# Optimization experiments

Hardware: AMD Instinct MI355X
Metric: run time of the kernel (lower is better)

The kernel has to match this reference:

```python
import jax, jax.numpy as jnp
import numpy as np
from jax import lax

EPS = 1e-6
DT_RANK = 24  # ceil(384/16), Mamba convention
D_STATE = 16


def _ln(x, g, b, eps=EPS):
    m = jnp.mean(x, axis=-1, keepdims=True)
    v = jnp.mean((x - m) ** 2, axis=-1, keepdims=True)
    return (x - m) * lax.rsqrt(v + eps) * g + b


def setup_inputs() -> dict:
    key = jax.random.key(0)
    ks = jax.random.split(key, 10)
    B, Dd, Hh, Ww, C = 2, 8, 16, 16, 384
    di, ds, r = 384, D_STATE, DT_RANK  # d_inner = expand * d_model = 384
    s = 0.02
    f = lambda k, shape: (jax.random.normal(k, shape, jnp.float32) * s)
    return {
        "x": jax.random.normal(ks[0], (B, Dd, Hh, Ww, C), jnp.float32),
        "g1": jnp.ones((C,), jnp.float32), "b1": jnp.zeros((C,), jnp.float32),
        "W_in": f(ks[1], (C, 2 * di)), "b_in": jnp.zeros((2 * di,), jnp.float32),
        "conv_w": f(ks[2], (di, 1, 3, 3, 3)), "conv_b": jnp.zeros((di,), jnp.float32),
        "W_x": f(ks[3], (di, r + 2 * ds)),
        "W_dt": f(ks[4], (r, di)), "b_dt": jnp.zeros((di,), jnp.float32),
        "A_log": jnp.tile(jnp.log(jnp.arange(1, ds + 1, dtype=jnp.float32)), (di, 1)),
        "D_skip": jnp.ones((di,), jnp.float32),
        "on_g": jnp.ones((di,), jnp.float32), "on_b": jnp.zeros((di,), jnp.float32),
        "W_out": f(ks[5], (di, C)), "b_out": jnp.zeros((C,), jnp.float32),
        "g2": jnp.ones((C,), jnp.float32), "b2": jnp.zeros((C,), jnp.float32),
        "W1": f(ks[6], (C, C)), "b1m": jnp.zeros((C,), jnp.float32),
        "W2": f(ks[7], (C, C)), "b2m": jnp.zeros((C,), jnp.float32),
    }


def _ss3d(h, W_in, b_in, conv_w, conv_b, W_x, W_dt, b_dt, A_log, D_skip, on_g, on_b, W_out, b_out):
    # h: [B, D, H, W, C] -> Mamba-style selective scan over flattened DHW (orientation 0)
    B, Dd, Hh, Ww, C = h.shape
    di = W_in.shape[1] // 2
    ds = D_STATE
    L = Dd * Hh * Ww
    seq = h.reshape(B, L, C)
    xz = seq @ W_in + b_in                      # [B, L, 2*di]
    xin, z = jnp.split(xz, 2, axis=-1)
    # depthwise 3D conv + SiLU on the x branch
    xc = xin.reshape(B, Dd, Hh, Ww, di).transpose(0, 4, 1, 2, 3)  # [B, di, D, H, W]
    xc = lax.conv_general_dilated(xc, conv_w, (1, 1, 1), 'SAME',
                                  feature_group_count=di,
                                  dimension_numbers=('NCDHW', 'OIDHW', 'NCDHW'))
    xc = xc + conv_b[None, :, None, None, None]
    xin = jax.nn.silu(xc).transpose(0, 2, 3, 4, 1).reshape(B, L, di)
    # input-dependent dt, B, C
    dbc = xin @ W_x                              # [B, L, r + 2*ds]
    dt, Bm, Cm = jnp.split(dbc, [DT_RANK, DT_RANK + ds], axis=-1)
    dt = jax.nn.softplus(dt @ W_dt + b_dt)       # [B, L, di]
    A = -jnp.exp(A_log)                          # [di, ds]
    dA = jnp.exp(dt[..., None] * A)              # [B, L, di, ds]
    dBx = dt[..., None] * Bm[:, :, None, :] * xin[..., None]  # [B, L, di, ds]

    def step(carry, inp):
        da, dbx, c = inp                         # [B,di,ds], [B,di,ds], [B,ds]
        carry = da * carry + dbx
        y = jnp.einsum('bds,bs->bd', carry, c)
        return carry, y

    xs = (dA.transpose(1, 0, 2, 3), dBx.transpose(1, 0, 2, 3), Cm.transpose(1, 0, 2))
    h0 = jnp.zeros((B, di, ds), dA.dtype)
    _, ys = lax.scan(step, h0, xs)               # ys: [L, B, di]
    y = ys.transpose(1, 0, 2) + xin * D_skip
    y = _ln(y, on_g, on_b) * jax.nn.silu(z)
    out = y @ W_out + b_out
    return out.reshape(B, Dd, Hh, Ww, C)


def reference(x, g1, b1, W_in, b_in, conv_w, conv_b, W_x, W_dt, b_dt, A_log, D_skip,
              on_g, on_b, W_out, b_out, g2, b2, W1, b1m, W2, b2m):
    # x + SS3D(LN(x)); then x + MLP(LN(x)).  drop_path/dropout = 0 (eval)
    a = _ss3d(_ln(x, g1, b1), W_in, b_in, conv_w, conv_b, W_x, W_dt, b_dt,
              A_log, D_skip, on_g, on_b, W_out, b_out)
    x1 = x + a
    h2 = _ln(x1, g2, b2)
    mlp = jax.nn.gelu(h2 @ W1 + b1m) @ W2 + b2m
    return x1 + mlp
```

## Files before the change

### kernel.cpp

```cpp
#include <hip/hip_runtime.h>
#include <hip/hip_bf16.h>

using bf16 = __hip_bfloat16;
#define DEV __device__ __forceinline__

typedef __attribute__((ext_vector_type(8))) short short8;
typedef __attribute__((ext_vector_type(8))) unsigned short ushort8;
typedef __attribute__((ext_vector_type(4))) float f32x4;

constexpr int Bb = 2, DD = 8, HH = 16, WW = 16;
constexpr int C = 384, DI = 384, DS = 16, RR = 24;
constexpr int L = DD * HH * WW;
constexpr int M = Bb * L;

DEV bf16 f2b(float v) { return __float2bfloat16(v); }
DEV unsigned short f2bu(float v) {
    bf16 t = __float2bfloat16(v);
    unsigned short u; __builtin_memcpy(&u, &t, 2); return u;
}
DEV float braw(unsigned short u) {
    unsigned int x = ((unsigned int)u) << 16;
    float f; __builtin_memcpy(&f, &x, 4); return f;
}
DEV bool isbf(const unsigned short* g1p) { return g1p[0] == 0x3F80; }

typedef const __attribute__((address_space(1))) unsigned int* gaddr_t;
typedef __attribute__((address_space(3))) unsigned int* laddr_t;
DEV void gload_lds16(const void* g, void* l) {
    __builtin_amdgcn_global_load_lds((gaddr_t)g, (laddr_t)l, 16, 0, 0);
}

DEV float wred64(float v) {
    #pragma unroll
    for (int off = 32; off > 0; off >>= 1) v += __shfl_xor(v, off, 64);
    return v;
}
DEV float siluf(float x) { return x / (1.0f + __expf(-x)); }
DEV float softplusf(float x) { return (x > 15.0f) ? x : log1pf(__expf(x)); }
DEV float gelu_tanh(float x) {
    const float k0 = 0.7978845608028654f;
    float u = k0 * (x + 0.044715f * x * x * x);
    float e = __expf(2.0f * u);
    float t = 1.0f - 2.0f / (e + 1.0f);
    return 0.5f * x * (1.0f + t);
}

struct PrepTab {
    const void* tsrc[4];
    unsigned short* tdst[4];
    int tK[4], tN[4];
    const void* csrc[17];
    float* cdst[17];
    int coff[18];
};
__global__ __launch_bounds__(256) void prep_k(PrepTab t,
                                              const unsigned short* __restrict__ g1p,
                                              int ctotal) {
    bool fl = isbf(g1p);
    int z = blockIdx.z;
    if (z < 4) {
        __shared__ unsigned short tt[32][33];
        int N = t.tN[z], K = t.tK[z];
        int n0 = blockIdx.x * 32, k0 = blockIdx.y * 32;
        if (n0 >= N || k0 >= K) return;
        const void* src = t.tsrc[z];
        unsigned short* dst = t.tdst[z];
        int tx = threadIdx.x & 31, ty = threadIdx.x >> 5;
        #pragma unroll
        for (int i = 0; i < 4; i++) {
            int k = k0 + ty + i * 8;
            unsigned short u;
            if (fl) u = ((const unsigned short*)src)[(size_t)k * N + n0 + tx];
            else    u = f2bu(((const float*)src)[(size_t)k * N + n0 + tx]);
            tt[ty + i * 8][tx] = u;
        }
        __syncthreads();
        #pragma unroll
        for (int i = 0; i < 4; i++) {
            int n = n0 + ty + i * 8;
            dst[(size_t)n * K + k0 + tx] = tt[tx][ty + i * 8];
        }
    } else {
        int i = (blockIdx.y * 24 + blockIdx.x) * 256 + threadIdx.x;
        if (i >= ctotal) return;
        int seg = 0;
        #pragma unroll
        for (int k = 1; k < 18; k++) seg += (i >= t.coff[k]) ? 1 : 0;
        int j = i - t.coff[seg];
        const void* s = t.csrc[seg];
        float v = fl ? braw(((const unsigned short*)s)[j]) : ((const float*)s)[j];
        t.cdst[seg][j] = v;
    }
}

template <bool RAWIN>
__global__ __launch_bounds__(256) void ln_k(const void* __restrict__ xr,
                                            const float* __restrict__ g,
                                            const float* __restrict__ b,
                                            bf16* __restrict__ out,
                                            const unsigned short* __restrict__ g1p) {
    bool fl = RAWIN ? isbf(g1p) : false;
    int wave = blockIdx.x * 4 + (threadIdx.x >> 6);
    int lane = threadIdx.x & 63;
    size_t base = (size_t)wave * C;
    float v[6];
    #pragma unroll
    for (int j = 0; j < 6; j++) {
        size_t idx = base + lane + 64 * j;
        if (RAWIN && fl) v[j] = braw(((const unsigned short*)xr)[idx]);
        else             v[j] = ((const float*)xr)[idx];
    }
    float s = 0.f;
    #pragma unroll
    for (int j = 0; j < 6; j++) s += v[j];
    s = wred64(s);
    float mean = s * (1.0f / C);
    float q = 0.f;
    #pragma unroll
    for (int j = 0; j < 6; j++) { float d = v[j] - mean; q += d * d; }
    q = wred64(q);
    float rstd = rsqrtf(q * (1.0f / C) + 1e-6f);
    #pragma unroll
    for (int j = 0; j < 6; j++) {
        int c = lane + 64 * j;
        out[base + c] = f2b((v[j] - mean) * rstd * g[c] + b[c]);
    }
}

enum { EPI_XZT = 0, EPI_OUT = 1, EPI_GELU = 2, EPI_FINAL = 3 };

template <int N, int TN, int EPI>
__global__ __launch_bounds__(256) void gemm_mfma(const bf16* __restrict__ A,
                                                 const unsigned short* __restrict__ Bt,
                                                 const float* __restrict__ bias,
                                                 float* __restrict__ o0,
                                                 float* __restrict__ o1,
                                                 const float* __restrict__ auxf,
                                                 const void* __restrict__ auxraw,
                                                 void* __restrict__ obf,
                                                 const unsigned short* __restrict__ g1p) {
    __shared__ unsigned short Asb[128 * 32];
    __shared__ unsigned short Bsb[TN * 32];
    constexpr int MT = (TN == 128) ? 4 : 2;
    int tid = threadIdx.x;
    int m0 = blockIdx.x * 128, n0 = blockIdx.y * TN;
    int wid = tid >> 6, lane = tid & 63;
    int wm = (TN == 128) ? (wid >> 1) * 64 : wid * 32;
    int wn = (TN == 128) ? (wid & 1) * 64 : 0;
    int quad = lane >> 4, l15 = lane & 15;
    f32x4 acc[MT][4] = {};
    int srow = tid >> 2, sseg = (tid & 3) * 8;
    const unsigned short* Au = (const unsigned short*)A;
    for (int k0 = 0; k0 < 384; k0 += 32) {
        __syncthreads();
        gload_lds16(Au + (size_t)(m0 + srow) * 384 + k0 + sseg,
                    &Asb[srow * 32 + sseg]);
        gload_lds16(Au + (size_t)(m0 + 64 + srow) * 384 + k0 + sseg,
                    &Asb[(64 + srow) * 32 + sseg]);
        gload_lds16(Bt + (size_t)(n0 + srow) * 384 + k0 + sseg,
                    &Bsb[srow * 32 + sseg]);
        if constexpr (TN == 128)
            gload_lds16(Bt + (size_t)(n0 + 64 + srow) * 384 + k0 + sseg,
                        &Bsb[(64 + srow) * 32 + sseg]);
        __syncthreads();
        short8 af[MT], bfr[4];
        #pragma unroll
        for (int mt = 0; mt < MT; mt++)
            af[mt] = *(const short8*)&Asb[(wm + mt * 16 + l15) * 32 + quad * 8];
        #pragma unroll
        for (int nt = 0; nt < 4; nt++)
            bfr[nt] = *(const short8*)&Bsb[(wn + nt * 16 + l15) * 32 + quad * 8];
        #pragma unroll
        for (int mt = 0; mt < MT; mt++)
            #pragma unroll
            for (int nt = 0; nt < 4; nt++)
                acc[mt][nt] = __builtin_amdgcn_mfma_f32_16x16x32_bf16(
                    af[mt], bfr[nt], acc[mt][nt], 0, 0, 0);
    }
    bool fl = (EPI == EPI_FINAL || EPI == EPI_OUT) ? isbf(g1p) : false;
    #pragma unroll
    for (int mt = 0; mt < MT; mt++) {
        #pragma unroll
        for (int nt = 0; nt < 4; nt++) {
            int n = n0 + wn + nt * 16 + l15;
            int mb = m0 + wm + mt * 16 + quad * 4;
            float bi = bias[n];
            if constexpr (EPI == EPI_XZT) {
                f32x4 v = acc[mt][nt];
                v[0] += bi; v[1] += bi; v[2] += bi; v[3] += bi;
                float* dst = (n < 384) ? (o0 + (size_t)n * M + mb)
                                       : (o1 + (size_t)(n - 384) * M + mb);
                *(f32x4*)dst = v;
            } else {
                #pragma unroll
                for (int r = 0; r < 4; r++) {
                    int m = mb + r;
                    float v = acc[mt][nt][r] + bi;
                    if constexpr (EPI == EPI_OUT) {
                        float av;
                        if (fl) av = braw(((const unsigned short*)auxraw)[(size_t)m * 384 + n]);
                        else    av = ((const float*)auxraw)[(size_t)m * 384 + n];
                        o0[(size_t)m * 384 + n] = v + av;
                    } else if constexpr (EPI == EPI_GELU) {
                        ((bf16*)obf)[(size_t)m * 384 + n] = f2b(gelu_tanh(v));
                    } else {
                        float rr = v + auxf[(size_t)m * 384 + n];
                        if (fl) ((bf16*)obf)[(size_t)m * 384 + n] = f2b(rr);
                        else    ((float*)obf)[(size_t)m * 384 + n] = rr;
                    }
                }
            }
        }
    }
}

__global__ __launch_bounds__(256) void convT_k(const float* __restrict__ xT,
                                               const float* __restrict__ cw,
                                               const float* __restrict__ cb,
                                               float* __restrict__ xinT) {
    int c = blockIdx.y;
    int m0 = (blockIdx.x * 256 + threadIdx.x) * 4;
    int l = m0 & (L - 1);
    int d = l >> 8, h = (l >> 4) & 15, w0 = l & 15;
    const float* xc = xT + (size_t)c * M;
    const float* wc = cw + c * 27;
    float bias = cb[c];
    float acc[4] = {bias, bias, bias, bias};
    #pragma unroll
    for (int kd = -1; kd <= 1; kd++) {
        int dd = d + kd; if ((unsigned)dd >= 8u) continue;
        #pragma unroll
        for (int kh = -1; kh <= 1; kh++) {
            int hh = h + kh; if ((unsigned)hh >= 16u) continue;
            int mm = m0 + kd * 256 + kh * 16;
            float vv[6];
            vv[0] = (w0 == 0) ? 0.f : xc[mm - 1];
            float4 v14 = *(const float4*)(xc + mm);
            vv[1] = v14.x; vv[2] = v14.y; vv[3] = v14.z; vv[4] = v14.w;
            vv[5] = (w0 == 12) ? 0.f : xc[mm + 4];
            const float* wk = wc + (kd + 1) * 9 + (kh + 1) * 3;
            float wa = wk[0], wb = wk[1], wcc = wk[2];
            #pragma unroll
            for (int j = 0; j < 4; j++)
                acc[j] = fmaf(vv[j], wa, fmaf(vv[j + 1], wb, fmaf(vv[j + 2], wcc, acc[j])));
        }
    }
    float4 o = make_float4(siluf(acc[0]), siluf(acc[1]), siluf(acc[2]), siluf(acc[3]));
    *(float4*)(xinT + (size_t)c * M + m0) = o;
}

__global__ __launch_bounds__(256) void dbc2_k(const float* __restrict__ xinT,
                                              const float* __restrict__ Wx,
                                              float* __restrict__ part) {
    __shared__ float As[16][64];
    __shared__ float Ws[16 * 56];
    int tid = threadIdx.x;
    int m0 = blockIdx.x * 64;
    int kc = blockIdx.y;
    int tm = tid & 63, grp = tid >> 6;
    int kk = tid >> 4, mc = (tid & 15) * 4;
    float acc[14] = {};
    for (int k0 = kc * 64; k0 < kc * 64 + 64; k0 += 16) {
        float4 av = *(const float4*)(xinT + (size_t)(k0 + kk) * M + m0 + mc);
        __syncthreads();
        *(float4*)&As[kk][mc] = av;
        for (int idx = tid; idx < 16 * 56; idx += 256)
            Ws[idx] = Wx[k0 * 56 + idx];
        __syncthreads();
        #pragma unroll
        for (int k = 0; k < 16; k++) {
            float a = As[k][tm];
            #pragma unroll
            for (int jj = 0; jj < 14; jj++)
                acc[jj] = fmaf(a, Ws[k * 56 + grp * 14 + jj], acc[jj]);
        }
    }
    int m = m0 + tm;
    #pragma unroll
    for (int jj = 0; jj < 14; jj++) {
        int col = grp * 14 + jj;
        part[((size_t)kc * 56 + col) * M + m] = acc[jj];
    }
}

__global__ __launch_bounds__(256) void dbcred_k(const float* __restrict__ part,
                                                float* __restrict__ dtrT,
                                                unsigned short* __restrict__ Brow,
                                                unsigned short* __restrict__ Crow) {
    int col = blockIdx.y;
    int m = blockIdx.x * 256 + threadIdx.x;
    float s = 0.f;
    #pragma unroll
    for (int kc = 0; kc < 6; kc++)
        s += part[((size_t)kc * 56 + col) * M + m];
    if (col < 24)      dtrT[(size_t)col * M + m] = s;
    else if (col < 40) Brow[(size_t)m * 16 + col - 24] = f2bu(s);
    else               Crow[(size_t)m * 16 + col - 40] = f2bu(s);
}

__global__ __launch_bounds__(256) void dtT_k(const float* __restrict__ dtrT,
                                             const float* __restrict__ Wdt,
                                             const float* __restrict__ bdt,
                                             float* __restrict__ dtT) {
    int lane = threadIdx.x & 63;
    int wv = threadIdx.x >> 6;
    int n = blockIdx.y * 4 + wv;
    int m = blockIdx.x * 64 + lane;
    float acc = bdt[n];
    #pragma unroll
    for (int j = 0; j < 24; j++)
        acc = fmaf(dtrT[(size_t)j * M + m], Wdt[j * 384 + n], acc);
    dtT[(size_t)n * M + m] = softplusf(acc);
}

__global__ __launch_bounds__(128) void scan4_k(const float* __restrict__ dtT,
                                               const float* __restrict__ xinT,
                                               const unsigned short* __restrict__ Brow,
                                               const unsigned short* __restrict__ Crow,
                                               const float* __restrict__ alog,
                                               const float* __restrict__ dsk,
                                               float* __restrict__ yT) {
    __shared__ float dt_s[2112], x_s[2112];
    __shared__ float ypart[2 * 2112];
    int bi = blockIdx.x;
    int b = bi / DI, d = bi % DI;
    int wave = threadIdx.x >> 6, lane = threadIdx.x & 63;
    int s0 = wave * 8;
    float Aneg[8];
    #pragma unroll
    for (int ss = 0; ss < 8; ss++) Aneg[ss] = -__expf(alog[d * DS + s0 + ss]);
    const float* dtp = dtT + (size_t)d * M + b * L;
    const float* xp  = xinT + (size_t)d * M + b * L;
    #pragma unroll
    for (int i = 0; i < 4; i++) {
        int t4 = (threadIdx.x + i * 128) * 4;
        float4 dv = *(const float4*)(dtp + t4);
        float4 xv = *(const float4*)(xp + t4);
        int base = t4 + (t4 >> 5);
        dt_s[base + 0] = dv.x; dt_s[base + 1] = dv.y;
        dt_s[base + 2] = dv.z; dt_s[base + 3] = dv.w;
        x_s[base + 0] = xv.x; x_s[base + 1] = xv.y;
        x_s[base + 2] = xv.z; x_s[base + 3] = xv.w;
    }
    __syncthreads();
    const unsigned short* Bp = Brow + ((size_t)b * L) * 16 + s0;
    const unsigned short* Cp = Crow + ((size_t)b * L) * 16 + s0;
    int tbase = lane * 32;
    int pbase = lane * 33;
    float Ap[8], Bg[8];
    #pragma unroll
    for (int ss = 0; ss < 8; ss++) { Ap[ss] = 1.f; Bg[ss] = 0.f; }
    #pragma unroll 4
    for (int j = 0; j < 32; j++) {
        float dtv = dt_s[pbase + j];
        float dxv = dtv * x_s[pbase + j];
        ushort8 bu = *(const ushort8*)(Bp + (size_t)(tbase + j) * 16);
        #pragma unroll
        for (int ss = 0; ss < 8; ss++) {
            float dA = __expf(dtv * Aneg[ss]);
            Bg[ss] = fmaf(dA, Bg[ss], dxv * braw(bu[ss]));
            Ap[ss] *= dA;
        }
    }
    float carry[8];
    #pragma unroll
    for (int ss = 0; ss < 8; ss++) {
        float a = Ap[ss], bb = Bg[ss];
        #pragma unroll
        for (int off = 1; off < 64; off <<= 1) {
            float ap = __shfl_up(a, off, 64);
            float bp = __shfl_up(bb, off, 64);
            if (lane >= off) { bb = fmaf(a, bp, bb); a *= ap; }
        }
        float c = __shfl_up(bb, 1, 64);
        carry[ss] = (lane == 0) ? 0.f : c;
    }
    float* ypw = ypart + wave * 2112;
    float h[8];
    #pragma unroll
    for (int ss = 0; ss < 8; ss++) h[ss] = carry[ss];
    #pragma unroll 4
    for (int j = 0; j < 32; j++) {
        float dtv = dt_s[pbase + j];
        float dxv = dtv * x_s[pbase + j];
        size_t toff = (size_t)(tbase + j) * 16;
        ushort8 bu = *(const ushort8*)(Bp + toff);
        ushort8 cu = *(const ushort8*)(Cp + toff);
        float acc = 0.f;
        #pragma unroll
        for (int ss = 0; ss < 8; ss++) {
            float dA = __expf(dtv * Aneg[ss]);
            h[ss] = fmaf(dA, h[ss], dxv * braw(bu[ss]));
            acc = fmaf(h[ss], braw(cu[ss]), acc);
        }
        ypw[pbase + j] = acc;
    }
    __syncthreads();
    float Dv = dsk[d];
    float* yp = yT + (size_t)d * M + b * L;
    #pragma unroll
    for (int i = 0; i < 16; i++) {
        int t = threadIdx.x + 128 * i;
        int ti = t + (t >> 5);
        yp[t] = fmaf(x_s[ti], Dv, ypart[ti] + ypart[2112 + ti]);
    }
}

__global__ __launch_bounds__(256) void lnmulT_k(const float* __restrict__ yT,
                                                const float* __restrict__ zT,
                                                const float* __restrict__ g,
                                                const float* __restrict__ b,
                                                unsigned short* __restrict__ yact) {
    __shared__ float rs1[8][32], rs2[8][32];
    __shared__ float meanb[32], rstdb[32];
    __shared__ unsigned short tile[32][392];
    int moff = threadIdx.x & 31;
    int dsub = threadIdx.x >> 5;
    int m0 = blockIdx.x * 32;
    size_t mg = m0 + moff;
    float s1 = 0.f, s2 = 0.f;
    #pragma unroll 8
    for (int j = 0; j < 48; j++) {
        int d = dsub + 8 * j;
        float v = yT[(size_t)d * M + mg];
        s1 += v; s2 += v * v;
    }
    rs1[dsub][moff] = s1;
    rs2[dsub][moff] = s2;
    __syncthreads();
    if (threadIdx.x < 32) {
        float a1 = 0.f, a2 = 0.f;
        #pragma unroll
        for (int ss = 0; ss < 8; ss++) { a1 += rs1[ss][threadIdx.x]; a2 += rs2[ss][threadIdx.x]; }
        float mean = a1 * (1.0f / DI);
        float var = a2 * (1.0f / DI) - mean * mean;
        meanb[threadIdx.x] = mean;
        rstdb[threadIdx.x] = rsqrtf(var + 1e-6f);
    }
    __syncthreads();
    float mean = meanb[moff], rstd = rstdb[moff];
    #pragma unroll 8
    for (int j = 0; j < 48; j++) {
        int d = dsub + 8 * j;
        float v = yT[(size_t)d * M + mg];
        float ln = (v - mean) * rstd * g[d] + b[d];
        float zv = zT[(size_t)d * M + mg];
        tile[moff][d] = f2bu(ln * siluf(zv));
    }
    __syncthreads();
    #pragma unroll
    for (int i = 0; i < 6; i++) {
        int chunk = threadIdx.x + 256 * i;
        int row = chunk / 48, cc = chunk % 48;
        *(uint4*)(yact + ((size_t)(m0 + row)) * 384 + cc * 8) =
            *(const uint4*)&tile[row][cc * 8];
    }
}

extern "C" void kernel_launch(void* const* d_in, const int* in_sizes, int n_in,
                              void* d_out, int out_size, void* d_ws, size_t ws_size,
                              hipStream_t stream) {
    float* ws = (float*)d_ws;
    constexpr size_t S = (size_t)M * 384;
    bf16*  hb   = (bf16*)ws;
    float* xT   = ws + S / 2;
    float* zT   = xT + S;
    float* xinT = zT + S;
    float* dtT  = xinT + S;
    float* x1   = dtT + S;
    float* dtrT = x1 + S;
    unsigned short* Brow = (unsigned short*)(dtrT + (size_t)24 * M);
    unsigned short* Crow = Brow + (size_t)M * 16;
    float* part = (float*)(Crow + (size_t)M * 16);
    float* smalls = part + (size_t)6 * 56 * M;

    float* g1f  = smalls;        float* b1f  = g1f + 384;
    float* binf = b1f + 384;     float* cwf  = binf + 768;
    float* cbf  = cwf + 10368;   float* wxf  = cbf + 384;
    float* wdtf = wxf + 21504;   float* bdtf = wdtf + 9216;
    float* alogf= bdtf + 384;    float* dskf = alogf + 6144;
    float* ongf = dskf + 384;    float* onbf = ongf + 384;
    float* boutf= onbf + 384;    float* g2f  = boutf + 384;
    float* b2f_ = g2f + 384;     float* b1mf = b2f_ + 384;
    float* b2mf = b1mf + 384;
    unsigned short* WinT  = (unsigned short*)(b2mf + 384);
    unsigned short* WoutT = WinT + 294912;
    unsigned short* W1T   = WoutT + 147456;
    unsigned short* W2T   = W1T + 147456;

    float* yT = xT;
    bf16* h2b = hb;
    unsigned short* yactb = (unsigned short*)dtT;
    unsigned short* m1b = (unsigned short*)zT;
    const unsigned short* g1p = (const unsigned short*)d_in[1];

    PrepTab tab;
    {
        tab.tsrc[0] = d_in[3];  tab.tdst[0] = WinT;  tab.tK[0] = 384; tab.tN[0] = 768;
        tab.tsrc[1] = d_in[14]; tab.tdst[1] = WoutT; tab.tK[1] = 384; tab.tN[1] = 384;
        tab.tsrc[2] = d_in[18]; tab.tdst[2] = W1T;   tab.tK[2] = 384; tab.tN[2] = 384;
        tab.tsrc[3] = d_in[20]; tab.tdst[3] = W2T;   tab.tK[3] = 384; tab.tN[3] = 384;
        int idxs[17] = {1, 2, 4, 5, 6, 7, 8, 9, 10, 11, 12, 13, 15, 16, 17, 19, 21};
        float* dsts[17] = {g1f, b1f, binf, cwf, cbf, wxf, wdtf, bdtf, alogf, dskf,
                           ongf, onbf, boutf, g2f, b2f_, b1mf, b2mf};
        int ns[17] = {384, 384, 768, 10368, 384, 21504, 9216, 384, 6144, 384,
                      384, 384, 384, 384, 384, 384, 384};
        int off = 0;
        for (int k = 0; k < 17; k++) {
            tab.csrc[k] = d_in[idxs[k]];
            tab.cdst[k] = dsts[k];
            tab.coff[k] = off;
            off += ns[k];
        }
        tab.coff[17] = off;
        prep_k<<<dim3(24, 12, 5), 256, 0, stream>>>(tab, g1p, off);
    }

    ln_k<true><<<M / 4, 256, 0, stream>>>(d_in[0], g1f, b1f, hb, g1p);
    gemm_mfma<768, 128, EPI_XZT><<<dim3(M / 128, 6), 256, 0, stream>>>(
        hb, WinT, binf, xT, zT, nullptr, nullptr, nullptr, g1p);
    convT_k<<<dim3(M / 1024, DI), 256, 0, stream>>>(xT, cwf, cbf, xinT);
    dbc2_k<<<dim3(M / 64, 6), 256, 0, stream>>>(xinT, wxf, part);
    dbcred_k<<<dim3(M / 256, 56), 256, 0, stream>>>(part, dtrT, Brow, Crow);
    dtT_k<<<dim3(M / 64, DI / 4), 256, 0, stream>>>(dtrT, wdtf, bdtf, dtT);
    scan4_k<<<Bb * DI, 128, 0, stream>>>(dtT, xinT, Brow, Crow, alogf, dskf, yT);
    lnmulT_k<<<M / 32, 256, 0, stream>>>(yT, zT, ongf, onbf, yactb);
    gemm_mfma<384, 64, EPI_OUT><<<dim3(M / 128, 6), 256, 0, stream>>>(
        (const bf16*)yactb, WoutT, boutf, x1, nullptr, nullptr, d_in[0], nullptr, g1p);
    ln_k<false><<<M / 4, 256, 0, stream>>>(x1, g2f, b2f_, h2b, g1p);
    gemm_mfma<384, 64, EPI_GELU><<<dim3(M / 128, 6), 256, 0, stream>>>(
        h2b, W1T, b1mf, nullptr, nullptr, nullptr, nullptr, m1b, g1p);
    gemm_mfma<384, 64, EPI_FINAL><<<dim3(M / 128, 6), 256, 0, stream>>>(
        (const bf16*)m1b, W2T, b2mf, nullptr, nullptr, x1, nullptr, d_out, g1p);
}
```

Before: 230.6 us.

## Fuse LayerNorms into following GEMMs and merge dt reduction with dt projection

Removes both standalone LayerNorm kernels. Each GEMM that consumes normalized activations now computes per-row mean and rstd for its 128-row tile, then normalizes and converts the A operand to bf16 while staging it into shared memory. The split-K reduction of the x-projection partials is merged with the dt projection and softplus into one kernel, which drops the dtrT intermediate buffer and two kernel launches. In exchange, every N-tile block recomputes the row statistics and rereads the fp32 A rows (6x redundant reads). The A-tile loads are also now synchronous register loads instead of direct-to-LDS loads.

```diff
diff --git a/kernel.cpp b/kernel.cpp
--- a/kernel.cpp
+++ b/kernel.cpp
@@ -93,48 +93,131 @@
     }
 }
 
-template <bool RAWIN>
-__global__ __launch_bounds__(256) void ln_k(const void* __restrict__ xr,
-                                            const float* __restrict__ g,
-                                            const float* __restrict__ b,
-                                            bf16* __restrict__ out,
-                                            const unsigned short* __restrict__ g1p) {
-    bool fl = RAWIN ? isbf(g1p) : false;
-    int wave = blockIdx.x * 4 + (threadIdx.x >> 6);
-    int lane = threadIdx.x & 63;
-    size_t base = (size_t)wave * C;
-    float v[6];
-    #pragma unroll
-    for (int j = 0; j < 6; j++) {
-        size_t idx = base + lane + 64 * j;
-        if (RAWIN && fl) v[j] = braw(((const unsigned short*)xr)[idx]);
-        else             v[j] = ((const float*)xr)[idx];
-    }
-    float s = 0.f;
-    #pragma unroll
-    for (int j = 0; j < 6; j++) s += v[j];
-    s = wred64(s);
-    float mean = s * (1.0f / C);
-    float q = 0.f;
-    #pragma unroll
-    for (int j = 0; j < 6; j++) { float d = v[j] - mean; q += d * d; }
-    q = wred64(q);
-    float rstd = rsqrtf(q * (1.0f / C) + 1e-6f);
-    #pragma unroll
-    for (int j = 0; j < 6; j++) {
-        int c = lane + 64 * j;
-        out[base + c] = f2b((v[j] - mean) * rstd * g[c] + b[c]);
-    }
-}
-
 enum { EPI_XZT = 0, EPI_OUT = 1, EPI_GELU = 2, EPI_FINAL = 3 };
+
+template <int N, int TN, int EPI, bool ARAW>
+__global__ __launch_bounds__(256) void lngemm_k(const void* __restrict__ Ar,
+                                                const float* __restrict__ g,
+                                                const float* __restrict__ b,
+                                                const unsigned short* __restrict__ Bt,
+                                                const float* __restrict__ bias,
+                                                float* __restrict__ o0,
+                                                float* __restrict__ o1,
+                                                void* __restrict__ obf,
+                                                const unsigned short* __restrict__ g1p) {
+    __shared__ unsigned short Asb[128 * 32];
+    __shared__ unsigned short Bsb[TN * 32];
+    __shared__ float mean_s[128], rstd_s[128];
+    __shared__ float gb[768];
+    constexpr int MT = (TN == 128) ? 4 : 2;
+    int tid = threadIdx.x;
+    int m0 = blockIdx.x * 128, n0 = blockIdx.y * TN;
+    int wid = tid >> 6, lane = tid & 63;
+    bool fl = ARAW ? isbf(g1p) : false;
+    for (int i = tid; i < 384; i += 256) { gb[i] = g[i]; gb[384 + i] = b[i]; }
+    for (int r = 0; r < 32; r++) {
+        int row = m0 + wid * 32 + r;
+        float v[6];
+        #pragma unroll
+        for (int j = 0; j < 6; j++) {
+            size_t idx = (size_t)row * 384 + lane + 64 * j;
+            if (ARAW && fl) v[j] = braw(((const unsigned short*)Ar)[idx]);
+            else            v[j] = ((const float*)Ar)[idx];
+        }
+        float s = 0.f;
+        #pragma unroll
+        for (int j = 0; j < 6; j++) s += v[j];
+        s = wred64(s);
+        float mean = s * (1.0f / 384.0f);
+        float q = 0.f;
+        #pragma unroll
+        for (int j = 0; j < 6; j++) { float d = v[j] - mean; q += d * d; }
+        q = wred64(q);
+        if (lane == 0) {
+            mean_s[wid * 32 + r] = mean;
+            rstd_s[wid * 32 + r] = rsqrtf(q * (1.0f / 384.0f) + 1e-6f);
+        }
+    }
+    int wm = (TN == 128) ? (wid >> 1) * 64 : wid * 32;
+    int wn = (TN == 128) ? (wid & 1) * 64 : 0;
+    int quad = lane >> 4, l15 = lane & 15;
+    f32x4 acc[MT][4] = {};
+    int srow = tid >> 2, sseg = (tid & 3) * 8;
+    for (int k0 = 0; k0 < 384; k0 += 32) {
+        __syncthreads();
+        #pragma unroll
+        for (int half = 0; half < 2; half++) {
+            int r = srow + half * 64;
+            size_t off = (size_t)(m0 + r) * 384 + k0 + sseg;
+            float vals[8];
+            if (ARAW && fl) {
+                uint4 u = *(const uint4*)((const unsigned short*)Ar + off);
+                unsigned short us[8]; __builtin_memcpy(us, &u, 16);
+                #pragma unroll
+                for (int j = 0; j < 8; j++) vals[j] = braw(us[j]);
+            } else {
+                float4 f0 = *(const float4*)((const float*)Ar + off);
+                float4 f1 = *(const float4*)((const float*)Ar + off + 4);
+                vals[0] = f0.x; vals[1] = f0.y; vals[2] = f0.z; vals[3] = f0.w;
+                vals[4] = f1.x; vals[5] = f1.y; vals[6] = f1.z; vals[7] = f1.w;
+            }
+            float mn = mean_s[r], rs = rstd_s[r];
+            unsigned short ou[8];
+            #pragma unroll
+            for (int j = 0; j < 8; j++)
+                ou[j] = f2bu((vals[j] - mn) * rs * gb[k0 + sseg + j] + gb[384 + k0 + sseg + j]);
+            uint4 pk; __builtin_memcpy(&pk, ou, 16);
+            *(uint4*)&Asb[r * 32 + sseg] = pk;
+        }
+        gload_lds16(Bt + (size_t)(n0 + srow) * 384 + k0 + sseg, &Bsb[srow * 32 + sseg]);
+        if constexpr (TN == 128)
+            gload_lds16(Bt + (size_t)(n0 + 64 + srow) * 384 + k0 + sseg,
+                        &Bsb[(64 + srow) * 32 + sseg]);
+        __syncthreads();
+        short8 af[MT], bfr[4];
+        #pragma unroll
+        for (int mt = 0; mt < MT; mt++)
+            af[mt] = *(const short8*)&Asb[(wm + mt * 16 + l15) * 32 + quad * 8];
+        #pragma unroll
+        for (int nt = 0; nt < 4; nt++)
+            bfr[nt] = *(const short8*)&Bsb[(wn + nt * 16 + l15) * 32 + quad * 8];
+        #pragma unroll
+        for (int mt = 0; mt < MT; mt++)
+            #pragma unroll
+            for (int nt = 0; nt < 4; nt++)
+                acc[mt][nt] = __builtin_amdgcn_mfma_f32_16x16x32_bf16(
+                    af[mt], bfr[nt], acc[mt][nt], 0, 0, 0);
+    }
+    #pragma unroll
+    for (int mt = 0; mt < MT; mt++) {
+        #pragma unroll
+        for (int nt = 0; nt < 4; nt++) {
+            int n = n0 + wn + nt * 16 + l15;
+            int mb = m0 + wm + mt * 16 + quad * 4;
+            float bi = bias[n];
+            if constexpr (EPI == EPI_XZT) {
+                f32x4 v = acc[mt][nt];
+                v[0] += bi; v[1] += bi; v[2] += bi; v[3] += bi;
+                float* dst = (n < 384) ? (o0 + (size_t)n * M + mb)
+                                       : (o1 + (size_t)(n - 384) * M + mb);
+                *(f32x4*)dst = v;
+            } else {
+                #pragma unroll
+                for (int r = 0; r < 4; r++) {
+                    int m = mb + r;
+                    float v = acc[mt][nt][r] + bi;
+                    ((bf16*)obf)[(size_t)m * 384 + n] = f2b(gelu_tanh(v));
+                }
+            }
+        }
+    }
+}
 
 template <int N, int TN, int EPI>
 __global__ __launch_bounds__(256) void gemm_mfma(const bf16* __restrict__ A,
                                                  const unsigned short* __restrict__ Bt,
                                                  const float* __restrict__ bias,
                                                  float* __restrict__ o0,
-                                                 float* __restrict__ o1,
                                                  const float* __restrict__ auxf,
                                                  const void* __restrict__ auxraw,
                                                  void* __restrict__ obf,
@@ -153,12 +236,10 @@
     const unsigned short* Au = (const unsigned short*)A;
     for (int k0 = 0; k0 < 384; k0 += 32) {
         __syncthreads();
-        gload_lds16(Au + (size_t)(m0 + srow) * 384 + k0 + sseg,
-                    &Asb[srow * 32 + sseg]);
+        gload_lds16(Au + (size_t)(m0 + srow) * 384 + k0 + sseg, &Asb[srow * 32 + sseg]);
         gload_lds16(Au + (size_t)(m0 + 64 + srow) * 384 + k0 + sseg,
                     &Asb[(64 + srow) * 32 + sseg]);
-        gload_lds16(Bt + (size_t)(n0 + srow) * 384 + k0 + sseg,
-                    &Bsb[srow * 32 + sseg]);
+        gload_lds16(Bt + (size_t)(n0 + srow) * 384 + k0 + sseg, &Bsb[srow * 32 + sseg]);
         if constexpr (TN == 128)
             gload_lds16(Bt + (size_t)(n0 + 64 + srow) * 384 + k0 + sseg,
                         &Bsb[(64 + srow) * 32 + sseg]);
@@ -177,7 +258,7 @@
                 acc[mt][nt] = __builtin_amdgcn_mfma_f32_16x16x32_bf16(
                     af[mt], bfr[nt], acc[mt][nt], 0, 0, 0);
     }
-    bool fl = (EPI == EPI_FINAL || EPI == EPI_OUT) ? isbf(g1p) : false;
+    bool fl = isbf(g1p);
     #pragma unroll
     for (int mt = 0; mt < MT; mt++) {
         #pragma unroll
@@ -185,29 +266,19 @@
             int n = n0 + wn + nt * 16 + l15;
             int mb = m0 + wm + mt * 16 + quad * 4;
             float bi = bias[n];
-            if constexpr (EPI == EPI_XZT) {
-                f32x4 v = acc[mt][nt];
-                v[0] += bi; v[1] += bi; v[2] += bi; v[3] += bi;
-                float* dst = (n < 384) ? (o0 + (size_t)n * M + mb)
-                                       : (o1 + (size_t)(n - 384) * M + mb);
-                *(f32x4*)dst = v;
-            } else {
-                #pragma unroll
-                for (int r = 0; r < 4; r++) {
-                    int m = mb + r;
-                    float v = acc[mt][nt][r] + bi;
-                    if constexpr (EPI == EPI_OUT) {
-                        float av;
-                        if (fl) av = braw(((const unsigned short*)auxraw)[(size_t)m * 384 + n]);
-                        else    av = ((const float*)auxraw)[(size_t)m * 384 + n];
-                        o0[(size_t)m * 384 + n] = v + av;
-                    } else if constexpr (EPI == EPI_GELU) {
-                        ((bf16*)obf)[(size_t)m * 384 + n] = f2b(gelu_tanh(v));
-                    } else {
-                        float rr = v + auxf[(size_t)m * 384 + n];
-                        if (fl) ((bf16*)obf)[(size_t)m * 384 + n] = f2b(rr);
-                        else    ((float*)obf)[(size_t)m * 384 + n] = rr;
-                    }
+            #pragma unroll
+            for (int r = 0; r < 4; r++) {
+                int m = mb + r;
+                float v = acc[mt][nt][r] + bi;
+                if constexpr (EPI == EPI_OUT) {
+                    float av;
+                    if (fl) av = braw(((const unsigned short*)auxraw)[(size_t)m * 384 + n]);
+                    else    av = ((const float*)auxraw)[(size_t)m * 384 + n];
+                    o0[(size_t)m * 384 + n] = v + av;
+                } else {
+                    float rr = v + auxf[(size_t)m * 384 + n];
+                    if (fl) ((bf16*)obf)[(size_t)m * 384 + n] = f2b(rr);
+                    else    ((float*)obf)[(size_t)m * 384 + n] = rr;
                 }
             }
         }
@@ -283,34 +354,47 @@
     }
 }
 
-__global__ __launch_bounds__(256) void dbcred_k(const float* __restrict__ part,
-                                                float* __restrict__ dtrT,
+__global__ __launch_bounds__(256) void dbcfin_k(const float* __restrict__ part,
+                                                const float* __restrict__ Wdt,
+                                                const float* __restrict__ bdt,
+                                                float* __restrict__ dtT,
                                                 unsigned short* __restrict__ Brow,
                                                 unsigned short* __restrict__ Crow) {
-    int col = blockIdx.y;
-    int m = blockIdx.x * 256 + threadIdx.x;
-    float s = 0.f;
-    #pragma unroll
-    for (int kc = 0; kc < 6; kc++)
-        s += part[((size_t)kc * 56 + col) * M + m];
-    if (col < 24)      dtrT[(size_t)col * M + m] = s;
-    else if (col < 40) Brow[(size_t)m * 16 + col - 24] = f2bu(s);
-    else               Crow[(size_t)m * 16 + col - 40] = f2bu(s);
-}
-
-__global__ __launch_bounds__(256) void dtT_k(const float* __restrict__ dtrT,
-                                             const float* __restrict__ Wdt,
-                                             const float* __restrict__ bdt,
-                                             float* __restrict__ dtT) {
-    int lane = threadIdx.x & 63;
-    int wv = threadIdx.x >> 6;
-    int n = blockIdx.y * 4 + wv;
-    int m = blockIdx.x * 64 + lane;
-    float acc = bdt[n];
-    #pragma unroll
-    for (int j = 0; j < 24; j++)
-        acc = fmaf(dtrT[(size_t)j * M + m], Wdt[j * 384 + n], acc);
-    dtT[(size_t)n * M + m] = softplusf(acc);
+    __shared__ float dtr[24][64];
+    int tid = threadIdx.x;
+    int m0 = blockIdx.x * 64;
+    int ng = blockIdx.y;
+    for (int i = tid; i < 24 * 64; i += 256) {
+        int col = i >> 6, mm = i & 63;
+        float s = 0.f;
+        #pragma unroll
+        for (int kc = 0; kc < 6; kc++)
+            s += part[((size_t)kc * 56 + col) * M + m0 + mm];
+        dtr[col][mm] = s;
+    }
+    if (ng == 0) {
+        for (int i = tid; i < 32 * 64; i += 256) {
+            int col = 24 + (i >> 6), mm = i & 63;
+            float s = 0.f;
+            #pragma unroll
+            for (int kc = 0; kc < 6; kc++)
+                s += part[((size_t)kc * 56 + col) * M + m0 + mm];
+            int m = m0 + mm;
+            if (col < 40) Brow[(size_t)m * 16 + col - 24] = f2bu(s);
+            else          Crow[(size_t)m * 16 + col - 40] = f2bu(s);
+        }
+    }
+    __syncthreads();
+    int mm = tid & 63, nq = tid >> 6;
+    #pragma unroll 4
+    for (int nj = 0; nj < 16; nj++) {
+        int n = ng * 64 + nq * 16 + nj;
+        float acc = bdt[n];
+        #pragma unroll
+        for (int j = 0; j < 24; j++)
+            acc = fmaf(dtr[j][mm], Wdt[j * 384 + n], acc);
+        dtT[(size_t)n * M + m0 + mm] = softplusf(acc);
+    }
 }
 
 __global__ __launch_bounds__(128) void scan4_k(const float* __restrict__ dtT,
@@ -462,14 +546,12 @@
                               hipStream_t stream) {
     float* ws = (float*)d_ws;
     constexpr size_t S = (size_t)M * 384;
-    bf16*  hb   = (bf16*)ws;
-    float* xT   = ws + S / 2;
+    float* xT   = ws;
     float* zT   = xT + S;
     float* xinT = zT + S;
     float* dtT  = xinT + S;
     float* x1   = dtT + S;
-    float* dtrT = x1 + S;
-    unsigned short* Brow = (unsigned short*)(dtrT + (size_t)24 * M);
+    unsigned short* Brow = (unsigned short*)(x1 + S);
     unsigned short* Crow = Brow + (size_t)M * 16;
     float* part = (float*)(Crow + (size_t)M * 16);
     float* smalls = part + (size_t)6 * 56 * M;
@@ -489,7 +571,6 @@
     unsigned short* W2T   = W1T + 147456;
 
     float* yT = xT;
-    bf16* h2b = hb;
     unsigned short* yactb = (unsigned short*)dtT;
     unsigned short* m1b = (unsigned short*)zT;
     const unsigned short* g1p = (const unsigned short*)d_in[1];
@@ -516,20 +597,17 @@
         prep_k<<<dim3(24, 12, 5), 256, 0, stream>>>(tab, g1p, off);
     }
 
-    ln_k<true><<<M / 4, 256, 0, stream>>>(d_in[0], g1f, b1f, hb, g1p);
-    gemm_mfma<768, 128, EPI_XZT><<<dim3(M / 128, 6), 256, 0, stream>>>(
-        hb, WinT, binf, xT, zT, nullptr, nullptr, nullptr, g1p);
+    lngemm_k<768, 128, EPI_XZT, true><<<dim3(M / 128, 6), 256, 0, stream>>>(
+        d_in[0], g1f, b1f, WinT, binf, xT, zT, nullptr, g1p);
     convT_k<<<dim3(M / 1024, DI), 256, 0, stream>>>(xT, cwf, cbf, xinT);
     dbc2_k<<<dim3(M / 64, 6), 256, 0, stream>>>(xinT, wxf, part);
-    dbcred_k<<<dim3(M / 256, 56), 256, 0, stream>>>(part, dtrT, Brow, Crow);
-    dtT_k<<<dim3(M / 64, DI / 4), 256, 0, stream>>>(dtrT, wdtf, bdtf, dtT);
+    dbcfin_k<<<dim3(M / 64, 6), 256, 0, stream>>>(part, wdtf, bdtf, dtT, Brow, Crow);
     scan4_k<<<Bb * DI, 128, 0, stream>>>(dtT, xinT, Brow, Crow, alogf, dskf, yT);
     lnmulT_k<<<M / 32, 256, 0, stream>>>(yT, zT, ongf, onbf, yactb);
     gemm_mfma<384, 64, EPI_OUT><<<dim3(M / 128, 6), 256, 0, stream>>>(
-        (const bf16*)yactb, WoutT, boutf, x1, nullptr, nullptr, d_in[0], nullptr, g1p);
-    ln_k<false><<<M / 4, 256, 0, stream>>>(x1, g2f, b2f_, h2b, g1p);
-    gemm_mfma<384, 64, EPI_GELU><<<dim3(M / 128, 6), 256, 0, stream>>>(
-        h2b, W1T, b1mf, nullptr, nullptr, nullptr, nullptr, m1b, g1p);
+        (const bf16*)yactb, WoutT, boutf, x1, nullptr, d_in[0], nullptr, g1p);
+    lngemm_k<384, 64, EPI_GELU, false><<<dim3(M / 128, 6), 256, 0, stream>>>(
+        x1, g2f, b2f_, W1T, b1mf, nullptr, nullptr, m1b, g1p);
     gemm_mfma<384, 64, EPI_FINAL><<<dim3(M / 128, 6), 256, 0, stream>>>(
-        (const bf16*)m1b, W2T, b2mf, nullptr, nullptr, x1, nullptr, d_out, g1p);
-}
+        (const bf16*)m1b, W2T, b2mf, nullptr, x1, nullptr, d_out, g1p);
+}
```

Result: slower. 280.5 us (+21.6%).
